# Performance work log

Measured on AMD Instinct MI355X. Metric: run time of the kernel, lower is better.

## Reference

```python
import jax, jax.numpy as jnp
import numpy as np

B, L, C, H, W = 2, 8, 64, 128, 128
HID = 256


def setup_inputs() -> dict:
    key = jax.random.key(0)
    k0, k1, k2, k3, k4 = jax.random.split(key, 5)
    x = jax.random.normal(k0, (B, L, C, H, W), dtype=jnp.float32)
    # Conv2d(in*4 -> hidden, kernel=1): weight stored as [out, in] for 1x1
    conv_w = jax.random.normal(k1, (HID, 4 * C), dtype=jnp.float32) * (1.0 / np.sqrt(4 * C))
    conv_b = jax.random.normal(k2, (HID,), dtype=jnp.float32) * 0.01
    conv_out_w = jax.random.normal(k3, (4 * C, HID), dtype=jnp.float32) * (1.0 / np.sqrt(HID))
    conv_out_b = jax.random.normal(k4, (4 * C,), dtype=jnp.float32) * 0.01
    return {"x": x, "conv_w": conv_w, "conv_b": conv_b,
            "conv_out_w": conv_out_w, "conv_out_b": conv_out_b}


def _dwt(x):  # x: [N, C, Hp, Wp] (even dims) -> [N, 4C, Hp/2, Wp/2]
    x1 = x[:, :, 0::2, 0::2] * 0.5
    x2 = x[:, :, 1::2, 0::2] * 0.5
    x3 = x[:, :, 0::2, 1::2] * 0.5
    x4 = x[:, :, 1::2, 1::2] * 0.5
    return jnp.concatenate([x1 + x2 + x3 + x4,
                            -x1 - x2 + x3 + x4,
                            -x1 + x2 - x3 + x4,
                            x1 - x2 - x3 + x4], axis=1)


def _idwt(y):  # y: [N, 4C, Hh, Wh] -> [N, C, 2Hh, 2Wh]
    n, c4, hh, wh = y.shape
    co = c4 // 4
    y1 = y[:, 0 * co:1 * co] * 0.5
    y2 = y[:, 1 * co:2 * co] * 0.5
    y3 = y[:, 2 * co:3 * co] * 0.5
    y4 = y[:, 3 * co:4 * co] * 0.5
    a = y1 - y2 - y3 + y4   # h[0::2, 0::2]
    b = y1 - y2 + y3 - y4   # h[1::2, 0::2]
    c = y1 + y2 - y3 - y4   # h[0::2, 1::2]
    d = y1 + y2 + y3 + y4   # h[1::2, 1::2]
    r0 = jnp.stack([a, c], axis=-1).reshape(n, co, hh, 2 * wh)  # even rows
    r1 = jnp.stack([b, d], axis=-1).reshape(n, co, hh, 2 * wh)  # odd rows
    return jnp.stack([r0, r1], axis=-2).reshape(n, co, 2 * hh, 2 * wh)


def reference(x, conv_w, conv_b, conv_out_w, conv_out_b):
    b, l, c, h, w = x.shape
    pad_h = (2 - h % 2) % 2
    pad_w = (2 - w % 2) % 2
    if pad_h > 0 or pad_w > 0:
        x = jnp.pad(x, ((0, 0), (0, 0), (0, 0), (0, pad_h), (0, pad_w)))
    hp, wp = x.shape[-2], x.shape[-1]
    xf = x.reshape(b * l, c, hp, wp)
    x_dwt = _dwt(xf)                                       # [BL, 4C, hp/2, wp/2]
    feat = jnp.einsum('nchw,oc->nohw', x_dwt, conv_w) + conv_b[None, :, None, None]
    feat = jax.nn.silu(feat)
    y = jnp.einsum('nchw,oc->nohw', feat, conv_out_w) + conv_out_b[None, :, None, None]
    rec = _idwt(y)                                         # [BL, C, hp, wp]
    out = rec.reshape(b, l, c, hp, wp)
    if pad_h > 0 or pad_w > 0:
        out = out[..., :h, :w]
    return out
```

## Files before the change

### kernel.cpp

```cpp
#include <hip/hip_runtime.h>
#include <hip/hip_bf16.h>


typedef __bf16 bf16x8 __attribute__((ext_vector_type(8)));
typedef float  f32x4  __attribute__((ext_vector_type(4)));

#define SP 264

__device__ __forceinline__ unsigned short f2bf(float f) {
  __hip_bfloat16 h = __float2bfloat16(f);
  return __builtin_bit_cast(unsigned short, h);
}
__device__ __forceinline__ float bf2f(unsigned short s) {
  union { unsigned int i; float f; } v; v.i = ((unsigned int)s) << 16; return v.f;
}
__device__ __forceinline__ float silu(float f) {
  return f / (1.0f + __expf(-f));
}
__device__ __forceinline__ bf16x8 ldw8(const float* __restrict__ p) {
  const float4 a = *(const float4*)p;
  const float4 b = *(const float4*)(p + 4);
  bf16x8 r;
  r[0] = (__bf16)a.x; r[1] = (__bf16)a.y; r[2] = (__bf16)a.z; r[3] = (__bf16)a.w;
  r[4] = (__bf16)b.x; r[5] = (__bf16)b.y; r[6] = (__bf16)b.z; r[7] = (__bf16)b.w;
  return r;
}

__global__ __launch_bounds__(256, 2)
void wavelet_fused(const float* __restrict__ x,
                   const float* __restrict__ w1,
                   const float* __restrict__ b1,
                   const float* __restrict__ w2,
                   const float* __restrict__ b2,
                   float* __restrict__ out)
{
  __shared__ unsigned short ldsA[64 * SP];
  __shared__ unsigned short ldsB[64 * SP];

  const int t  = threadIdx.x;
  const int n  = blockIdx.x >> 6;
  const int hh = blockIdx.x & 63;

  const int ww = t & 63;
  const int cg = t >> 6;

  {
    const float* xb = x + ((size_t)n * 64 * 128 + (size_t)(2 * hh)) * 128 + 2 * ww;
    #pragma unroll
    for (int j = 0; j < 4; ++j) {
      const int c0 = (cg + 4 * j) * 4;
      float qv[4][4];
      #pragma unroll
      for (int ci = 0; ci < 4; ++ci) {
        const float* p = xb + (size_t)(c0 + ci) * (128 * 128);
        const float2 r0 = *(const float2*)p;
        const float2 r1 = *(const float2*)(p + 128);
        const float x1 = r0.x, x3 = r0.y;
        const float x2 = r1.x, x4 = r1.y;
        qv[0][ci] = 0.5f * ((x1 + x2) + (x3 + x4));
        qv[1][ci] = 0.5f * ((x3 + x4) - (x1 + x2));
        qv[2][ci] = 0.5f * ((x2 + x4) - (x1 + x3));
        qv[3][ci] = 0.5f * ((x1 + x4) - (x2 + x3));
      }
      #pragma unroll
      for (int q = 0; q < 4; ++q) {
        ushort4 v = make_ushort4(f2bf(qv[q][0]), f2bf(qv[q][1]), f2bf(qv[q][2]), f2bf(qv[q][3]));
        *(ushort4*)(&ldsA[ww * SP + q * 64 + c0]) = v;
      }
    }
  }
  __syncthreads();

  const int wv   = t >> 6;
  const int r    = t & 15;
  const int quad = (t & 63) >> 4;

  {
    f32x4 acc[4][4];
    #pragma unroll
    for (int mt = 0; mt < 4; ++mt)
      #pragma unroll
      for (int nt = 0; nt < 4; ++nt)
        acc[mt][nt] = (f32x4){0.0f, 0.0f, 0.0f, 0.0f};

    const float* wA = w1 + (wv * 64 + r) * 256 + quad * 8;
    #pragma unroll
    for (int k0 = 0; k0 < 256; k0 += 32) {
      bf16x8 a[4], b[4];
      #pragma unroll
      for (int mt = 0; mt < 4; ++mt)
        a[mt] = ldw8(wA + mt * (16 * 256) + k0);
      #pragma unroll
      for (int nt = 0; nt < 4; ++nt)
        b[nt] = *(const bf16x8*)(&ldsA[(nt * 16 + r) * SP + quad * 8 + k0]);
      #pragma unroll
      for (int mt = 0; mt < 4; ++mt)
        #pragma unroll
        for (int nt = 0; nt < 4; ++nt)
          acc[mt][nt] = __builtin_amdgcn_mfma_f32_16x16x32_bf16(a[mt], b[nt], acc[mt][nt], 0, 0, 0);
    }

    #pragma unroll
    for (int mt = 0; mt < 4; ++mt) {
      const int ob = wv * 64 + mt * 16 + quad * 4;
      const float4 bb = *(const float4*)(b1 + ob);
      #pragma unroll
      for (int nt = 0; nt < 4; ++nt) {
        const int pix = nt * 16 + r;
        ushort4 v;
        v.x = f2bf(silu(acc[mt][nt][0] + bb.x));
        v.y = f2bf(silu(acc[mt][nt][1] + bb.y));
        v.z = f2bf(silu(acc[mt][nt][2] + bb.z));
        v.w = f2bf(silu(acc[mt][nt][3] + bb.w));
        *(ushort4*)(&ldsB[pix * SP + ob]) = v;
      }
    }
  }
  __syncthreads();

  {
    f32x4 acc[4][4];
    #pragma unroll
    for (int mt = 0; mt < 4; ++mt)
      #pragma unroll
      for (int nt = 0; nt < 4; ++nt)
        acc[mt][nt] = (f32x4){0.0f, 0.0f, 0.0f, 0.0f};

    const float* wA = w2 + (wv * 64 + r) * 256 + quad * 8;
    #pragma unroll
    for (int k0 = 0; k0 < 256; k0 += 32) {
      bf16x8 a[4], b[4];
      #pragma unroll
      for (int mt = 0; mt < 4; ++mt)
        a[mt] = ldw8(wA + mt * (16 * 256) + k0);
      #pragma unroll
      for (int nt = 0; nt < 4; ++nt)
        b[nt] = *(const bf16x8*)(&ldsB[(nt * 16 + r) * SP + quad * 8 + k0]);
      #pragma unroll
      for (int mt = 0; mt < 4; ++mt)
        #pragma unroll
        for (int nt = 0; nt < 4; ++nt)
          acc[mt][nt] = __builtin_amdgcn_mfma_f32_16x16x32_bf16(a[mt], b[nt], acc[mt][nt], 0, 0, 0);
    }

    #pragma unroll
    for (int mt = 0; mt < 4; ++mt) {
      const int cb = wv * 64 + mt * 16 + quad * 4;
      const float4 bb = *(const float4*)(b2 + cb);
      #pragma unroll
      for (int nt = 0; nt < 4; ++nt) {
        const int pix = nt * 16 + r;
        ushort4 v;
        v.x = f2bf(acc[mt][nt][0] + bb.x);
        v.y = f2bf(acc[mt][nt][1] + bb.y);
        v.z = f2bf(acc[mt][nt][2] + bb.z);
        v.w = f2bf(acc[mt][nt][3] + bb.w);
        *(ushort4*)(&ldsA[pix * SP + cb]) = v;
      }
    }
  }
  __syncthreads();

  {
    float* ob_ = out + ((size_t)n * 64 * 128 + (size_t)(2 * hh)) * 128 + 2 * ww;
    #pragma unroll
    for (int j = 0; j < 4; ++j) {
      const int c0 = (cg + 4 * j) * 4;
      unsigned short yb[4][4];
      #pragma unroll
      for (int q = 0; q < 4; ++q) {
        const ushort4 v = *(const ushort4*)(&ldsA[ww * SP + q * 64 + c0]);
        yb[q][0] = v.x; yb[q][1] = v.y; yb[q][2] = v.z; yb[q][3] = v.w;
      }
      #pragma unroll
      for (int ci = 0; ci < 4; ++ci) {
        const float y1 = 0.5f * bf2f(yb[0][ci]);
        const float y2 = 0.5f * bf2f(yb[1][ci]);
        const float y3 = 0.5f * bf2f(yb[2][ci]);
        const float y4 = 0.5f * bf2f(yb[3][ci]);
        const float s14 = y1 + y4, s23 = y2 + y3;
        const float d14 = y1 - y4, d23 = y2 - y3;
        const float oa  = s14 - s23;
        const float oc  = d14 + d23;
        const float obv = d14 - d23;
        const float od  = s14 + s23;
        float* prow = ob_ + (size_t)(c0 + ci) * (128 * 128);
        *(float2*)prow         = make_float2(oa, oc);
        *(float2*)(prow + 128) = make_float2(obv, od);
      }
    }
  }
}

extern "C" void kernel_launch(void* const* d_in, const int* in_sizes, int n_in,
                              void* d_out, int out_size, void* d_ws, size_t ws_size,
                              hipStream_t stream) {
  (void)in_sizes; (void)n_in; (void)out_size; (void)d_ws; (void)ws_size;
  const float* x  = (const float*)d_in[0];
  const float* w1 = (const float*)d_in[1];
  const float* b1 = (const float*)d_in[2];
  const float* w2 = (const float*)d_in[3];
  const float* b2 = (const float*)d_in[4];
  float* o = (float*)d_out;
  wavelet_fused<<<dim3(16 * 64), dim3(256), 0, stream>>>(x, w1, b1, w2, b2, o);
}
```

Measured before the change: 179.6 us.

## Pre-convert weights to bf16 in workspace and share a single LDS buffer

```diff
diff --git a/kernel.cpp b/kernel.cpp
--- a/kernel.cpp
+++ b/kernel.cpp
@@ -26,16 +26,26 @@
   return r;
 }
 
-__global__ __launch_bounds__(256, 2)
+__global__ __launch_bounds__(256) void cvt_w(const float* __restrict__ w1,
+                                             const float* __restrict__ w2,
+                                             unsigned short* __restrict__ o) {
+  const int i = (blockIdx.x * 256 + threadIdx.x) * 4;
+  const float4 a = *(const float4*)(w1 + i);
+  const float4 b = *(const float4*)(w2 + i);
+  *(ushort4*)(o + i)         = make_ushort4(f2bf(a.x), f2bf(a.y), f2bf(a.z), f2bf(a.w));
+  *(ushort4*)(o + 65536 + i) = make_ushort4(f2bf(b.x), f2bf(b.y), f2bf(b.z), f2bf(b.w));
+}
+
+template <bool WBF16>
+__global__ __launch_bounds__(256, 4)
 void wavelet_fused(const float* __restrict__ x,
-                   const float* __restrict__ w1,
+                   const void* __restrict__ w1p,
                    const float* __restrict__ b1,
-                   const float* __restrict__ w2,
+                   const void* __restrict__ w2p,
                    const float* __restrict__ b2,
                    float* __restrict__ out)
 {
-  __shared__ unsigned short ldsA[64 * SP];
-  __shared__ unsigned short ldsB[64 * SP];
+  __shared__ unsigned short lds[64 * SP];
 
   const int t  = threadIdx.x;
   const int n  = blockIdx.x >> 6;
@@ -65,7 +75,7 @@
       #pragma unroll
       for (int q = 0; q < 4; ++q) {
         ushort4 v = make_ushort4(f2bf(qv[q][0]), f2bf(qv[q][1]), f2bf(qv[q][2]), f2bf(qv[q][3]));
-        *(ushort4*)(&ldsA[ww * SP + q * 64 + c0]) = v;
+        *(ushort4*)(&lds[ww * SP + q * 64 + c0]) = v;
       }
     }
   }
@@ -83,22 +93,27 @@
       for (int nt = 0; nt < 4; ++nt)
         acc[mt][nt] = (f32x4){0.0f, 0.0f, 0.0f, 0.0f};
 
-    const float* wA = w1 + (wv * 64 + r) * 256 + quad * 8;
     #pragma unroll
     for (int k0 = 0; k0 < 256; k0 += 32) {
       bf16x8 a[4], b[4];
       #pragma unroll
-      for (int mt = 0; mt < 4; ++mt)
-        a[mt] = ldw8(wA + mt * (16 * 256) + k0);
-      #pragma unroll
-      for (int nt = 0; nt < 4; ++nt)
-        b[nt] = *(const bf16x8*)(&ldsA[(nt * 16 + r) * SP + quad * 8 + k0]);
+      for (int mt = 0; mt < 4; ++mt) {
+        const int row = wv * 64 + mt * 16 + r;
+        if constexpr (WBF16)
+          a[mt] = *(const bf16x8*)((const unsigned short*)w1p + row * 256 + quad * 8 + k0);
+        else
+          a[mt] = ldw8((const float*)w1p + row * 256 + quad * 8 + k0);
+      }
+      #pragma unroll
+      for (int nt = 0; nt < 4; ++nt)
+        b[nt] = *(const bf16x8*)(&lds[(nt * 16 + r) * SP + quad * 8 + k0]);
       #pragma unroll
       for (int mt = 0; mt < 4; ++mt)
         #pragma unroll
         for (int nt = 0; nt < 4; ++nt)
           acc[mt][nt] = __builtin_amdgcn_mfma_f32_16x16x32_bf16(a[mt], b[nt], acc[mt][nt], 0, 0, 0);
     }
+    __syncthreads();
 
     #pragma unroll
     for (int mt = 0; mt < 4; ++mt) {
@@ -112,7 +127,7 @@
         v.y = f2bf(silu(acc[mt][nt][1] + bb.y));
         v.z = f2bf(silu(acc[mt][nt][2] + bb.z));
         v.w = f2bf(silu(acc[mt][nt][3] + bb.w));
-        *(ushort4*)(&ldsB[pix * SP + ob]) = v;
+        *(ushort4*)(&lds[pix * SP + ob]) = v;
       }
     }
   }
@@ -126,22 +141,27 @@
       for (int nt = 0; nt < 4; ++nt)
         acc[mt][nt] = (f32x4){0.0f, 0.0f, 0.0f, 0.0f};
 
-    const float* wA = w2 + (wv * 64 + r) * 256 + quad * 8;
     #pragma unroll
     for (int k0 = 0; k0 < 256; k0 += 32) {
       bf16x8 a[4], b[4];
       #pragma unroll
-      for (int mt = 0; mt < 4; ++mt)
-        a[mt] = ldw8(wA + mt * (16 * 256) + k0);
-      #pragma unroll
-      for (int nt = 0; nt < 4; ++nt)
-        b[nt] = *(const bf16x8*)(&ldsB[(nt * 16 + r) * SP + quad * 8 + k0]);
+      for (int mt = 0; mt < 4; ++mt) {
+        const int row = wv * 64 + mt * 16 + r;
+        if constexpr (WBF16)
+          a[mt] = *(const bf16x8*)((const unsigned short*)w2p + row * 256 + quad * 8 + k0);
+        else
+          a[mt] = ldw8((const float*)w2p + row * 256 + quad * 8 + k0);
+      }
+      #pragma unroll
+      for (int nt = 0; nt < 4; ++nt)
+        b[nt] = *(const bf16x8*)(&lds[(nt * 16 + r) * SP + quad * 8 + k0]);
       #pragma unroll
       for (int mt = 0; mt < 4; ++mt)
         #pragma unroll
         for (int nt = 0; nt < 4; ++nt)
           acc[mt][nt] = __builtin_amdgcn_mfma_f32_16x16x32_bf16(a[mt], b[nt], acc[mt][nt], 0, 0, 0);
     }
+    __syncthreads();
 
     #pragma unroll
     for (int mt = 0; mt < 4; ++mt) {
@@ -155,7 +175,7 @@
         v.y = f2bf(acc[mt][nt][1] + bb.y);
         v.z = f2bf(acc[mt][nt][2] + bb.z);
         v.w = f2bf(acc[mt][nt][3] + bb.w);
-        *(ushort4*)(&ldsA[pix * SP + cb]) = v;
+        *(ushort4*)(&lds[pix * SP + cb]) = v;
       }
     }
   }
@@ -169,7 +189,7 @@
       unsigned short yb[4][4];
       #pragma unroll
       for (int q = 0; q < 4; ++q) {
-        const ushort4 v = *(const ushort4*)(&ldsA[ww * SP + q * 64 + c0]);
+        const ushort4 v = *(const ushort4*)(&lds[ww * SP + q * 64 + c0]);
         yb[q][0] = v.x; yb[q][1] = v.y; yb[q][2] = v.z; yb[q][3] = v.w;
       }
       #pragma unroll
@@ -195,12 +215,21 @@
 extern "C" void kernel_launch(void* const* d_in, const int* in_sizes, int n_in,
                               void* d_out, int out_size, void* d_ws, size_t ws_size,
                               hipStream_t stream) {
-  (void)in_sizes; (void)n_in; (void)out_size; (void)d_ws; (void)ws_size;
+  (void)in_sizes; (void)n_in; (void)out_size;
   const float* x  = (const float*)d_in[0];
   const float* w1 = (const float*)d_in[1];
   const float* b1 = (const float*)d_in[2];
   const float* w2 = (const float*)d_in[3];
   const float* b2 = (const float*)d_in[4];
   float* o = (float*)d_out;
-  wavelet_fused<<<dim3(16 * 64), dim3(256), 0, stream>>>(x, w1, b1, w2, b2, o);
-}
+
+  if (ws_size >= 2u * 65536u * sizeof(unsigned short)) {
+    unsigned short* wb = (unsigned short*)d_ws;
+    cvt_w<<<dim3(64), dim3(256), 0, stream>>>(w1, w2, wb);
+    wavelet_fused<true><<<dim3(16 * 64), dim3(256), 0, stream>>>(
+        x, wb, b1, wb + 65536, b2, o);
+  } else {
+    wavelet_fused<false><<<dim3(16 * 64), dim3(256), 0, stream>>>(
+        x, w1, b1, w2, b2, o);
+  }
+}
```

Measured after the change: 154.8 us. -13.8%, faster.
